# Performance work log

Measured on AMD Instinct MI355X. Metric: run time of the kernel, lower is better.

The kernel has to match this reference:

```python
import jax, jax.numpy as jnp
import numpy as np

D = 768
B = 512

def setup_inputs() -> dict:
    key = jax.random.key(0)
    k1, k2, k3 = jax.random.split(key, 3)
    v_x = jax.random.normal(k1, (B, D), dtype=jnp.float32)
    s_x = jax.random.normal(k2, (B, D), dtype=jnp.float32)
    # nn.Linear(D*D, 2) weight (2, D*D), bias (2,)
    fc_w = jax.random.normal(k3, (2, D * D), dtype=jnp.float32) * 0.01
    fc_b = jnp.zeros((2,), dtype=jnp.float32)
    return {"v_x": v_x, "s_x": s_x, "fc_w": fc_w, "fc_b": fc_b}

def reference(v_x, s_x, fc_w, fc_b):
    d = v_x.shape[1]
    # Original: M[b,i,j] = v_x[b,i]*s_x[b,j]; logits = M_flat @ fc_w.T + fc_b.
    # Equivalent bilinear form avoiding the (B,d,d) intermediate:
    # logits[b,k] = sum_ij v[b,i] * s[b,j] * fc_w[k, i*d+j]
    W = fc_w.reshape(2, d, d)  # W[k,i,j]
    logits = jnp.einsum('bi,kij,bj->bk', v_x, W, s_x) + fc_b
    weights = jax.nn.softmax(logits, axis=-1)
    a = weights[:, 0:1]
    b = weights[:, 1:2]
    fused_x = a * v_x + b * s_x
    return fused_x
```

## Files before the change

### kernel.cpp

```cpp
#include <hip/hip_runtime.h>

#define D 768
#define B 512

typedef _Float16 half8 __attribute__((ext_vector_type(8)));
typedef float floatx4 __attribute__((ext_vector_type(4)));

__global__ __launch_bounds__(256)
void prep_kernel(const float* __restrict__ v_x,
                 const float* __restrict__ fc_w,
                 _Float16* __restrict__ WT,
                 _Float16* __restrict__ v16)
{
    __shared__ _Float16 tile[32 * 33];
    const int bid = blockIdx.x;
    const int t   = threadIdx.x;

    if (bid < 1152) {
        const int cls = bid / 576;
        const int r2  = bid % 576;
        const int kt  = r2 / 24;
        const int jt  = r2 % 24;
        const float* Wc = fc_w + (size_t)cls * D * D;
        const int r  = t >> 3;
        const int c4 = t & 7;
        float4 f = *reinterpret_cast<const float4*>(
            &Wc[(size_t)(kt * 32 + r) * D + jt * 32 + c4 * 4]);
        tile[r * 33 + c4 * 4 + 0] = (_Float16)f.x;
        tile[r * 33 + c4 * 4 + 1] = (_Float16)f.y;
        tile[r * 33 + c4 * 4 + 2] = (_Float16)f.z;
        tile[r * 33 + c4 * 4 + 3] = (_Float16)f.w;
        __syncthreads();
        alignas(8) _Float16 o[4];
#pragma unroll
        for (int e = 0; e < 4; ++e) o[e] = tile[(c4 * 4 + e) * 33 + r];
        *reinterpret_cast<short4*>(
            &WT[((size_t)cls * D + jt * 32 + r) * D + kt * 32 + c4 * 4]) =
            *reinterpret_cast<short4*>(o);
    } else {
        const int b2 = bid - 1152;
        const int base = b2 * 1024 + t * 4;
        float4 f = *reinterpret_cast<const float4*>(&v_x[base]);
        alignas(8) _Float16 o[4] = {(_Float16)f.x, (_Float16)f.y,
                                    (_Float16)f.z, (_Float16)f.w};
        *reinterpret_cast<short4*>(&v16[base]) = *reinterpret_cast<short4*>(o);
    }
}

#define BM 64
#define BN 128
#define KC 96
#define LROW 104
#define NJT 6
#define NPART 48

__global__ __launch_bounds__(256, 3)
void gemm_kernel(const _Float16* __restrict__ v16,
                 const _Float16* __restrict__ WT,
                 const float* __restrict__ s_x,
                 float* __restrict__ partial )
{
    __shared__ _Float16 Alds[BM * LROW];
    __shared__ _Float16 Blds[BN * LROW];
    __shared__ float    red[BM * 4];

    const int tid = threadIdx.x;
    const int jb  = blockIdx.x;
    const int b0  = blockIdx.y * BM;
    const int gz  = blockIdx.z;
    const int kc0 = gz * KC;

    const int w    = tid >> 6;
    const int lane = tid & 63;
    const int li   = lane & 15;
    const int g    = lane >> 4;

#pragma unroll
    for (int p = 0; p < 3; ++p) {
        int q   = tid + 256 * p;
        int row = q / 12, ksl = q % 12;
        half8 h = *reinterpret_cast<const half8*>(
            &v16[(size_t)(b0 + row) * D + kc0 + ksl * 8]);
        *reinterpret_cast<half8*>(&Alds[row * LROW + ksl * 8]) = h;
    }
    const _Float16* Wrow = WT + (size_t)jb * BN * D;
#pragma unroll
    for (int p = 0; p < 6; ++p) {
        int q   = tid + 256 * p;
        int row = q / 12, ksl = q % 12;
        half8 h = *reinterpret_cast<const half8*>(
            &Wrow[(size_t)row * D + kc0 + ksl * 8]);
        *reinterpret_cast<half8*>(&Blds[row * LROW + ksl * 8]) = h;
    }
    __syncthreads();

    floatx4 acc[4][2];
#pragma unroll
    for (int m = 0; m < 4; ++m)
#pragma unroll
        for (int n = 0; n < 2; ++n) acc[m][n] = {0.f, 0.f, 0.f, 0.f};

#pragma unroll
    for (int ks = 0; ks < KC / 32; ++ks) {
        half8 a[4], bf[2];
#pragma unroll
        for (int m = 0; m < 4; ++m)
            a[m] = *reinterpret_cast<const half8*>(
                &Alds[(m * 16 + li) * LROW + ks * 32 + g * 8]);
#pragma unroll
        for (int n = 0; n < 2; ++n)
            bf[n] = *reinterpret_cast<const half8*>(
                &Blds[(w * 32 + n * 16 + li) * LROW + ks * 32 + g * 8]);
#pragma unroll
        for (int m = 0; m < 4; ++m)
#pragma unroll
            for (int n = 0; n < 2; ++n)
                acc[m][n] = __builtin_amdgcn_mfma_f32_16x16x32_f16(
                    a[m], bf[n], acc[m][n], 0, 0, 0);
    }

    const int js  = (jb % NJT) * BN;
    const int cls = jb / NJT;
#pragma unroll
    for (int m = 0; m < 4; ++m)
#pragma unroll
        for (int r = 0; r < 4; ++r) {
            const int row = m * 16 + 4 * g + r;
            const float* sp = s_x + (size_t)(b0 + row) * D + js + w * 32 + li;
            float val = acc[m][0][r] * sp[0] + acc[m][1][r] * sp[16];
            val += __shfl_xor(val, 1);
            val += __shfl_xor(val, 2);
            val += __shfl_xor(val, 4);
            val += __shfl_xor(val, 8);
            if (li == 0) red[row * 4 + w] = val;
        }
    __syncthreads();
    if (tid < BM) {
        float4 rv = *reinterpret_cast<const float4*>(&red[tid * 4]);
        partial[(size_t)(b0 + tid) * (2 * NPART) + cls * NPART + gz * NJT + (jb % NJT)]
            = rv.x + rv.y + rv.z + rv.w;
    }
}

__global__ __launch_bounds__(192)
void fuse_kernel(const float* __restrict__ v_x,
                 const float* __restrict__ s_x,
                 const float* __restrict__ partial,
                 const float* __restrict__ fc_b,
                 float* __restrict__ out)
{
    __shared__ float slog[2];
    const int b    = blockIdx.x;
    const int t    = threadIdx.x;
    const int wave = t >> 6;
    const int lane = t & 63;

    if (wave < 2) {
        const float* P = partial + (size_t)b * (2 * NPART) + wave * NPART;
        float val = (lane < NPART) ? P[lane] : 0.f;
        val += __shfl_xor(val, 1);
        val += __shfl_xor(val, 2);
        val += __shfl_xor(val, 4);
        val += __shfl_xor(val, 8);
        val += __shfl_xor(val, 16);
        val += __shfl_xor(val, 32);
        if (lane == 0) slog[wave] = val + fc_b[wave];
    }
    __syncthreads();

    const float l0 = slog[0], l1 = slog[1];
    const float mx = fmaxf(l0, l1);
    const float e0 = __expf(l0 - mx);
    const float e1 = __expf(l1 - mx);
    const float inv = 1.f / (e0 + e1);
    const float wa = e0 * inv;
    const float wb = e1 * inv;

    const float4* v4 = reinterpret_cast<const float4*>(v_x + (size_t)b * D);
    const float4* s4 = reinterpret_cast<const float4*>(s_x + (size_t)b * D);
    float4* o4 = reinterpret_cast<float4*>((float*)out + (size_t)b * D);
    float4 vv = v4[t], ss = s4[t], oo;
    oo.x = wa * vv.x + wb * ss.x;
    oo.y = wa * vv.y + wb * ss.y;
    oo.z = wa * vv.z + wb * ss.z;
    oo.w = wa * vv.w + wb * ss.w;
    o4[t] = oo;
}

extern "C" void kernel_launch(void* const* d_in, const int* in_sizes, int n_in,
                              void* d_out, int out_size, void* d_ws, size_t ws_size,
                              hipStream_t stream) {
    const float* v_x  = (const float*)d_in[0];
    const float* s_x  = (const float*)d_in[1];
    const float* fc_w = (const float*)d_in[2];
    const float* fc_b = (const float*)d_in[3];
    float* out = (float*)d_out;

    char* ws = (char*)d_ws;
    _Float16* WT  = (_Float16*)(ws);
    _Float16* v16 = (_Float16*)(ws + (size_t)(1 << 22));
    float* partial = (float*)(ws + (size_t)(1 << 23));

    prep_kernel<<<1152 + 384, 256, 0, stream>>>(v_x, fc_w, WT, v16);

    dim3 g1(12, B / BM, 8);
    gemm_kernel<<<g1, 256, 0, stream>>>(v16, WT, s_x, partial);

    fuse_kernel<<<B, 192, 0, stream>>>(v_x, s_x, partial, fc_b, out);
}
```

Before: 79.99 us.

## Fuse fp32-to-fp16 conversion into GEMM loads and drop prep kernel

Removes the separate prep kernel that transposed and converted fc_w and v_x to fp16. The GEMM now reads fp32 fc_w directly in its natural row layout and swaps operand roles: s_x tiles become the A operand and W rows indexed by i become the B operand, with v_x applied in the epilogue. The transpose becomes unnecessary because contraction runs over j, which is contiguous. This saves a kernel launch and a full write/read pass of the fp16 weight copy, at the cost of doubling global read bytes per GEMM block for fp32 tiles and doing conversions inline.

```diff
diff --git a/kernel.cpp b/kernel.cpp
--- a/kernel.cpp
+++ b/kernel.cpp
@@ -5,47 +5,6 @@
 
 typedef _Float16 half8 __attribute__((ext_vector_type(8)));
 typedef float floatx4 __attribute__((ext_vector_type(4)));
-
-__global__ __launch_bounds__(256)
-void prep_kernel(const float* __restrict__ v_x,
-                 const float* __restrict__ fc_w,
-                 _Float16* __restrict__ WT,
-                 _Float16* __restrict__ v16)
-{
-    __shared__ _Float16 tile[32 * 33];
-    const int bid = blockIdx.x;
-    const int t   = threadIdx.x;
-
-    if (bid < 1152) {
-        const int cls = bid / 576;
-        const int r2  = bid % 576;
-        const int kt  = r2 / 24;
-        const int jt  = r2 % 24;
-        const float* Wc = fc_w + (size_t)cls * D * D;
-        const int r  = t >> 3;
-        const int c4 = t & 7;
-        float4 f = *reinterpret_cast<const float4*>(
-            &Wc[(size_t)(kt * 32 + r) * D + jt * 32 + c4 * 4]);
-        tile[r * 33 + c4 * 4 + 0] = (_Float16)f.x;
-        tile[r * 33 + c4 * 4 + 1] = (_Float16)f.y;
-        tile[r * 33 + c4 * 4 + 2] = (_Float16)f.z;
-        tile[r * 33 + c4 * 4 + 3] = (_Float16)f.w;
-        __syncthreads();
-        alignas(8) _Float16 o[4];
-#pragma unroll
-        for (int e = 0; e < 4; ++e) o[e] = tile[(c4 * 4 + e) * 33 + r];
-        *reinterpret_cast<short4*>(
-            &WT[((size_t)cls * D + jt * 32 + r) * D + kt * 32 + c4 * 4]) =
-            *reinterpret_cast<short4*>(o);
-    } else {
-        const int b2 = bid - 1152;
-        const int base = b2 * 1024 + t * 4;
-        float4 f = *reinterpret_cast<const float4*>(&v_x[base]);
-        alignas(8) _Float16 o[4] = {(_Float16)f.x, (_Float16)f.y,
-                                    (_Float16)f.z, (_Float16)f.w};
-        *reinterpret_cast<short4*>(&v16[base]) = *reinterpret_cast<short4*>(o);
-    }
-}
 
 #define BM 64
 #define BN 128
@@ -55,9 +14,10 @@
 #define NPART 48
 
 __global__ __launch_bounds__(256, 3)
-void gemm_kernel(const _Float16* __restrict__ v16,
-                 const _Float16* __restrict__ WT,
+void gemm_kernel(const _Float16* __restrict__ unused,
+                 const float* __restrict__ fc_w,
                  const float* __restrict__ s_x,
+                 const float* __restrict__ v_x,
                  float* __restrict__ partial )
 {
     __shared__ _Float16 Alds[BM * LROW];
@@ -68,7 +28,11 @@
     const int jb  = blockIdx.x;
     const int b0  = blockIdx.y * BM;
     const int gz  = blockIdx.z;
-    const int kc0 = gz * KC;
+    const int j0  = gz * KC;
+
+    const int cls   = jb / NJT;
+    const int it    = jb % NJT;
+    const int ibase = it * BN;
 
     const int w    = tid >> 6;
     const int lane = tid & 63;
@@ -76,21 +40,29 @@
     const int g    = lane >> 4;
 
 #pragma unroll
-    for (int p = 0; p < 3; ++p) {
-        int q   = tid + 256 * p;
-        int row = q / 12, ksl = q % 12;
-        half8 h = *reinterpret_cast<const half8*>(
-            &v16[(size_t)(b0 + row) * D + kc0 + ksl * 8]);
-        *reinterpret_cast<half8*>(&Alds[row * LROW + ksl * 8]) = h;
-    }
-    const _Float16* Wrow = WT + (size_t)jb * BN * D;
-#pragma unroll
     for (int p = 0; p < 6; ++p) {
         int q   = tid + 256 * p;
-        int row = q / 12, ksl = q % 12;
-        half8 h = *reinterpret_cast<const half8*>(
-            &Wrow[(size_t)row * D + kc0 + ksl * 8]);
-        *reinterpret_cast<half8*>(&Blds[row * LROW + ksl * 8]) = h;
+        int row = q / 24;
+        int c4  = q % 24;
+        float4 f = *reinterpret_cast<const float4*>(
+            &s_x[(size_t)(b0 + row) * D + j0 + c4 * 4]);
+        alignas(8) _Float16 h[4] = {(_Float16)f.x, (_Float16)f.y,
+                                    (_Float16)f.z, (_Float16)f.w};
+        *reinterpret_cast<short4*>(&Alds[row * LROW + c4 * 4]) =
+            *reinterpret_cast<short4*>(h);
+    }
+    const float* __restrict__ Wc = fc_w + (size_t)cls * D * D;
+#pragma unroll
+    for (int p = 0; p < 12; ++p) {
+        int q   = tid + 256 * p;
+        int row = q / 24;
+        int c4  = q % 24;
+        float4 f = *reinterpret_cast<const float4*>(
+            &Wc[(size_t)(ibase + row) * D + j0 + c4 * 4]);
+        alignas(8) _Float16 h[4] = {(_Float16)f.x, (_Float16)f.y,
+                                    (_Float16)f.z, (_Float16)f.w};
+        *reinterpret_cast<short4*>(&Blds[row * LROW + c4 * 4]) =
+            *reinterpret_cast<short4*>(h);
     }
     __syncthreads();
 
@@ -119,15 +91,13 @@
                     a[m], bf[n], acc[m][n], 0, 0, 0);
     }
 
-    const int js  = (jb % NJT) * BN;
-    const int cls = jb / NJT;
 #pragma unroll
     for (int m = 0; m < 4; ++m)
 #pragma unroll
         for (int r = 0; r < 4; ++r) {
             const int row = m * 16 + 4 * g + r;
-            const float* sp = s_x + (size_t)(b0 + row) * D + js + w * 32 + li;
-            float val = acc[m][0][r] * sp[0] + acc[m][1][r] * sp[16];
+            const float* vp = v_x + (size_t)(b0 + row) * D + ibase + w * 32 + li;
+            float val = acc[m][0][r] * vp[0] + acc[m][1][r] * vp[16];
             val += __shfl_xor(val, 1);
             val += __shfl_xor(val, 2);
             val += __shfl_xor(val, 4);
@@ -137,7 +107,7 @@
     __syncthreads();
     if (tid < BM) {
         float4 rv = *reinterpret_cast<const float4*>(&red[tid * 4]);
-        partial[(size_t)(b0 + tid) * (2 * NPART) + cls * NPART + gz * NJT + (jb % NJT)]
+        partial[(size_t)(b0 + tid) * (2 * NPART) + cls * NPART + gz * NJT + it]
             = rv.x + rv.y + rv.z + rv.w;
     }
 }
@@ -196,15 +166,10 @@
     const float* fc_b = (const float*)d_in[3];
     float* out = (float*)d_out;
 
-    char* ws = (char*)d_ws;
-    _Float16* WT  = (_Float16*)(ws);
-    _Float16* v16 = (_Float16*)(ws + (size_t)(1 << 22));
-    float* partial = (float*)(ws + (size_t)(1 << 23));
+    float* partial = (float*)d_ws;
 
-    prep_kernel<<<1152 + 384, 256, 0, stream>>>(v_x, fc_w, WT, v16);
-
-    dim3 g1(12, B / BM, 8);
-    gemm_kernel<<<g1, 256, 0, stream>>>(v16, WT, s_x, partial);
+    dim3 g1(2 * NJT, B / BM, 8);
+    gemm_kernel<<<g1, 256, 0, stream>>>(nullptr, fc_w, s_x, v_x, partial);
 
     fuse_kernel<<<B, 192, 0, stream>>>(v_x, s_x, partial, fc_b, out);
 }
```

New measurement: 78.24 us. -2.2%, faster.
